# Kernel tuning notes

Measured on AMD Instinct MI355X. Metric: run time of the kernel, lower is better.

The kernel has to match this reference:

```python
import jax, jax.numpy as jnp
import numpy as np

NUM_ROUTES = 12800   # 32 * 20 * 20
NUM_CAPS = 25
IN_CH = 8
OUT_CH = 64
BATCH = 8
NUM_ITERS = 3


def setup_inputs() -> dict:
    key = jax.random.key(0)
    kx, kw = jax.random.split(key)
    x = jax.random.normal(kx, (BATCH, NUM_ROUTES, IN_CH), dtype=jnp.float32)
    # W parameter: torch shape [1, R, C, O, I] -> store as [R, C, O, I]
    W = jax.random.normal(kw, (NUM_ROUTES, NUM_CAPS, OUT_CH, IN_CH), dtype=jnp.float32)
    return {"x": x, "W": W}


def _squash_elementwise(s):
    # Faithful to source: squared_norm sums over last dim of s_j which has size 1,
    # so squash acts elementwise: s^2 * s / ((1+s^2) * |s|) = s*|s|/(1+s^2).
    sq = s * s
    return sq * s / ((1.0 + sq) * jnp.sqrt(sq))


def reference(x, W):
    # u_hat[b,r,c,o] = sum_i W[r,c,o,i] * x[b,r,i]
    u_hat = jnp.einsum('rcoi,bri->brco', W, x)  # [B, R, C, O]
    b_ij = jnp.zeros((NUM_ROUTES, NUM_CAPS), dtype=x.dtype)
    v = None
    for it in range(NUM_ITERS):
        # legacy F.softmax on 4D [1,R,C,1] uses implicit dim=1 -> over routes
        c_ij = jax.nn.softmax(b_ij, axis=0)                  # [R, C]
        s = jnp.einsum('rc,brco->bco', c_ij, u_hat)          # [B, C, O]
        v = _squash_elementwise(s)
        if it < NUM_ITERS - 1:
            # agreement: <u_hat, v> per (b,r,c), then mean over batch
            a = jnp.einsum('brco,bco->brc', u_hat, v)
            b_ij = b_ij + jnp.mean(a, axis=0)
    # torch returns v_j.squeeze(1) with shape [B, C, O, 1]
    return v[..., None]
```

## Files before the change

kernel.cpp:

```cpp
#include <hip/hip_runtime.h>
#include <cstdint>
#include <cstddef>

#define RN 12800
#define CN 25
#define ON 64
#define IN_ 8
#define BN 8
#define SOUT (BN*CN*ON)

#define RPC 64
#define NRC (RN / RPC)
#define NFIN (BN * CN)

typedef float    f4x __attribute__((ext_vector_type(4)));
typedef uint32_t u4x __attribute__((ext_vector_type(4)));

__device__ __forceinline__ uint32_t pack_bf16(float a, float b) {
    uint32_t ua = __float_as_uint(a);
    uint32_t ub = __float_as_uint(b);
    ua = (ua + 0x7fffu + ((ua >> 16) & 1u)) >> 16;
    ub = (ub + 0x7fffu + ((ub >> 16) & 1u)) & 0xffff0000u;
    return ua | ub;
}
__device__ __forceinline__ float lo_bf16(uint32_t q) { return __uint_as_float(q << 16); }
__device__ __forceinline__ float hi_bf16(uint32_t q) { return __uint_as_float(q & 0xffff0000u); }
__device__ __forceinline__ float squashf(float s) { return s * fabsf(s) / (1.f + s * s); }

__global__ void __launch_bounds__(320, 6)
caps_pass0(const float* __restrict__ x, const float* __restrict__ W,
           float* __restrict__ Sp, uint32_t* __restrict__ U)
{
    __shared__ float xs[RPC][BN][IN_];
    const int chunk = blockIdx.y;
    const int r0 = chunk * RPC;

    for (int t = threadIdx.x; t < RPC * BN * 2; t += 320) {
        const int i4 = t & 1;
        const int rl = (t >> 1) & (RPC - 1);
        const int b  = t >> 7;
        const float4 val = *reinterpret_cast<const float4*>(
            x + (((size_t)b * RN + r0 + rl) * IN_) + i4 * 4);
        *reinterpret_cast<float4*>(&xs[rl][b][i4 * 4]) = val;
    }
    __syncthreads();

    const int wave = threadIdx.x >> 6;
    const int lane = threadIdx.x & 63;
    const int c = blockIdx.x * 5 + wave;

    float acc[BN];
    #pragma unroll
    for (int b = 0; b < BN; ++b) acc[b] = 0.f;

    #pragma unroll 2
    for (int rl = 0; rl < RPC; ++rl) {
        const int r = r0 + rl;
        const f4x* wp = reinterpret_cast<const f4x*>(
            W + ((((size_t)r * CN + c) * ON + lane) * IN_));
        const f4x w0 = __builtin_nontemporal_load(wp);
        const f4x w1 = __builtin_nontemporal_load(wp + 1);

        float u[BN];
        #pragma unroll
        for (int b = 0; b < BN; ++b) {
            const float4 xa = *reinterpret_cast<const float4*>(&xs[rl][b][0]);
            const float4 xb = *reinterpret_cast<const float4*>(&xs[rl][b][4]);
            u[b] = w0.x*xa.x + w0.y*xa.y + w0.z*xa.z + w0.w*xa.w
                 + w1.x*xb.x + w1.y*xb.y + w1.z*xb.z + w1.w*xb.w;
            acc[b] += u[b];
        }
        u4x q;
        q.x = pack_bf16(u[0], u[1]);
        q.y = pack_bf16(u[2], u[3]);
        q.z = pack_bf16(u[4], u[5]);
        q.w = pack_bf16(u[6], u[7]);
        __builtin_nontemporal_store(q, reinterpret_cast<u4x*>(
            U + (((size_t)r * CN + c) * ON + lane) * 4));
    }

    float* sp = Sp + (size_t)chunk * SOUT;
    #pragma unroll
    for (int b = 0; b < BN; ++b)
        sp[(b * CN + c) * ON + lane] = acc[b];
}

template<int MODE>
__global__ void __launch_bounds__(320, 6)
caps_passU(const uint32_t* __restrict__ U, const float* __restrict__ vin,
           const float* __restrict__ bin, float* __restrict__ bout,
           float* __restrict__ Sp, float* __restrict__ Zp)
{
    const int chunk = blockIdx.y;
    const int r0 = chunk * RPC;
    const int wave = threadIdx.x >> 6;
    const int lane = threadIdx.x & 63;
    const int c = blockIdx.x * 5 + wave;

    float vreg[BN];
    #pragma unroll
    for (int b = 0; b < BN; ++b)
        vreg[b] = vin[(b * CN + c) * ON + lane];

    float acc[BN];
    #pragma unroll
    for (int b = 0; b < BN; ++b) acc[b] = 0.f;
    float zacc = 0.f;

    #pragma unroll 2
    for (int rl = 0; rl < RPC; ++rl) {
        const int r = r0 + rl;
        const u4x q = __builtin_nontemporal_load(reinterpret_cast<const u4x*>(
            U + (((size_t)r * CN + c) * ON + lane) * 4));
        float u[BN];
        u[0] = lo_bf16(q.x); u[1] = hi_bf16(q.x);
        u[2] = lo_bf16(q.y); u[3] = hi_bf16(q.y);
        u[4] = lo_bf16(q.z); u[5] = hi_bf16(q.z);
        u[6] = lo_bf16(q.w); u[7] = hi_bf16(q.w);

        float p = 0.f;
        #pragma unroll
        for (int b = 0; b < BN; ++b) p += u[b] * vreg[b];
        #pragma unroll
        for (int off = 32; off > 0; off >>= 1) p += __shfl_xor(p, off, 64);

        float bn = p * (1.0f / BN);
        if (MODE == 2) bn += bin[(size_t)r * CN + c];
        if (MODE == 1 && lane == 0) bout[(size_t)r * CN + c] = bn;
        const float e = __expf(bn);
        zacc += e;
        #pragma unroll
        for (int b = 0; b < BN; ++b) acc[b] += e * u[b];
    }

    float* sp = Sp + (size_t)chunk * SOUT;
    #pragma unroll
    for (int b = 0; b < BN; ++b)
        sp[(b * CN + c) * ON + lane] = acc[b];
    if (lane == 0)
        Zp[chunk * 32 + c] = zacc;
}

template<int PASS>
__global__ void __launch_bounds__(320)
caps_fin(const float* __restrict__ Sp, const float* __restrict__ Zp,
         float* __restrict__ vout)
{
    __shared__ float red[320];
    const int wu = blockIdx.x;
    const int t = threadIdx.x, lane = t & 63, g = t >> 6;
    const int c = wu % CN;

    float z = (float)RN;
    if (PASS >= 1) {
        float zp = 0.f;
        for (int j = lane; j < NRC; j += 64) zp += Zp[j * 32 + c];
        #pragma unroll
        for (int off = 32; off > 0; off >>= 1) zp += __shfl_xor(zp, off, 64);
        z = zp;
    }
    const int base = wu * ON + lane;
    float s = 0.f;
    for (int ch = g * 40; ch < g * 40 + 40; ++ch)
        s += Sp[(size_t)ch * SOUT + base];
    red[t] = s;
    __syncthreads();
    if (g == 0) {
        float ss = red[lane] + red[64 + lane] + red[128 + lane]
                 + red[192 + lane] + red[256 + lane];
        ss /= z;
        vout[base] = squashf(ss);
    }
}

extern "C" void kernel_launch(void* const* d_in, const int* in_sizes, int n_in,
                              void* d_out, int out_size, void* d_ws, size_t ws_size,
                              hipStream_t stream)
{
    const float* x = (const float*)d_in[0];
    const float* W = (const float*)d_in[1];
    float* out = (float*)d_out;
    float* ws = (float*)d_ws;

    float* v  = ws;
    float* b1 = v + SOUT;
    float* Zp = b1 + (size_t)RN * CN;
    float* Sp = Zp + (size_t)NRC * 32;
    uint32_t* U = (uint32_t*)(Sp + (size_t)NRC * SOUT);

    dim3 blk(320), grid(5, NRC), fg(NFIN);

    caps_pass0<<<grid, blk, 0, stream>>>(x, W, Sp, U);
    caps_fin<0><<<fg, blk, 0, stream>>>(Sp, Zp, v);
    caps_passU<1><<<grid, blk, 0, stream>>>(U, v, nullptr, b1, Sp, Zp);
    caps_fin<1><<<fg, blk, 0, stream>>>(Sp, Zp, v);
    caps_passU<2><<<grid, blk, 0, stream>>>(U, v, b1, nullptr, Sp, Zp);
    caps_fin<2><<<fg, blk, 0, stream>>>(Sp, Zp, out);
}
```

Measured before the change: 360.3 us.

## Make U capsule-major and batch four route loads per iteration

Reorders the bf16 u_hat intermediate so it is indexed capsule-major ([C][R][O]) instead of route-major. Each wave's sweep over consecutive routes then reads contiguous memory. Both the producing and consuming kernels now issue four route loads up front before computing, to raise memory-level parallelism. The pass0 occupancy hint drops from 6 to 4 waves per SIMD to make room for the extra registers, which may reduce latency hiding.

```diff
diff --git a/kernel.cpp b/kernel.cpp
--- a/kernel.cpp
+++ b/kernel.cpp
@@ -27,7 +27,9 @@
 __device__ __forceinline__ float hi_bf16(uint32_t q) { return __uint_as_float(q & 0xffff0000u); }
 __device__ __forceinline__ float squashf(float s) { return s * fabsf(s) / (1.f + s * s); }
 
-__global__ void __launch_bounds__(320, 6)
+#define UIDX(c, r, lane) ((((size_t)(c) * RN + (r)) * ON + (lane)) * 4)
+
+__global__ void __launch_bounds__(320, 4)
 caps_pass0(const float* __restrict__ x, const float* __restrict__ W,
            float* __restrict__ Sp, uint32_t* __restrict__ U)
 {
@@ -53,30 +55,40 @@
     #pragma unroll
     for (int b = 0; b < BN; ++b) acc[b] = 0.f;
 
-    #pragma unroll 2
-    for (int rl = 0; rl < RPC; ++rl) {
-        const int r = r0 + rl;
-        const f4x* wp = reinterpret_cast<const f4x*>(
-            W + ((((size_t)r * CN + c) * ON + lane) * IN_));
-        const f4x w0 = __builtin_nontemporal_load(wp);
-        const f4x w1 = __builtin_nontemporal_load(wp + 1);
-
-        float u[BN];
-        #pragma unroll
-        for (int b = 0; b < BN; ++b) {
-            const float4 xa = *reinterpret_cast<const float4*>(&xs[rl][b][0]);
-            const float4 xb = *reinterpret_cast<const float4*>(&xs[rl][b][4]);
-            u[b] = w0.x*xa.x + w0.y*xa.y + w0.z*xa.z + w0.w*xa.w
-                 + w1.x*xb.x + w1.y*xb.y + w1.z*xb.z + w1.w*xb.w;
-            acc[b] += u[b];
-        }
-        u4x q;
-        q.x = pack_bf16(u[0], u[1]);
-        q.y = pack_bf16(u[2], u[3]);
-        q.z = pack_bf16(u[4], u[5]);
-        q.w = pack_bf16(u[6], u[7]);
-        __builtin_nontemporal_store(q, reinterpret_cast<u4x*>(
-            U + (((size_t)r * CN + c) * ON + lane) * 4));
+    for (int rg = 0; rg < RPC; rg += 4) {
+        f4x wv[8];
+        #pragma unroll
+        for (int j = 0; j < 4; ++j) {
+            const int r = r0 + rg + j;
+            const f4x* wp = reinterpret_cast<const f4x*>(
+                W + ((((size_t)r * CN + c) * ON + lane) * IN_));
+            wv[2 * j]     = __builtin_nontemporal_load(wp);
+            wv[2 * j + 1] = __builtin_nontemporal_load(wp + 1);
+        }
+        u4x qv[4];
+        #pragma unroll
+        for (int j = 0; j < 4; ++j) {
+            const int rl = rg + j;
+            float u[BN];
+            #pragma unroll
+            for (int b = 0; b < BN; ++b) {
+                const float4 xa = *reinterpret_cast<const float4*>(&xs[rl][b][0]);
+                const float4 xb = *reinterpret_cast<const float4*>(&xs[rl][b][4]);
+                u[b] = wv[2*j].x*xa.x + wv[2*j].y*xa.y + wv[2*j].z*xa.z + wv[2*j].w*xa.w
+                     + wv[2*j+1].x*xb.x + wv[2*j+1].y*xb.y + wv[2*j+1].z*xb.z + wv[2*j+1].w*xb.w;
+                acc[b] += u[b];
+            }
+            qv[j].x = pack_bf16(u[0], u[1]);
+            qv[j].y = pack_bf16(u[2], u[3]);
+            qv[j].z = pack_bf16(u[4], u[5]);
+            qv[j].w = pack_bf16(u[6], u[7]);
+        }
+        #pragma unroll
+        for (int j = 0; j < 4; ++j) {
+            const int r = r0 + rg + j;
+            __builtin_nontemporal_store(qv[j],
+                reinterpret_cast<u4x*>(U + UIDX(c, r, lane)));
+        }
     }
 
     float* sp = Sp + (size_t)chunk * SOUT;
@@ -107,30 +119,36 @@
     for (int b = 0; b < BN; ++b) acc[b] = 0.f;
     float zacc = 0.f;
 
-    #pragma unroll 2
-    for (int rl = 0; rl < RPC; ++rl) {
-        const int r = r0 + rl;
-        const u4x q = __builtin_nontemporal_load(reinterpret_cast<const u4x*>(
-            U + (((size_t)r * CN + c) * ON + lane) * 4));
-        float u[BN];
-        u[0] = lo_bf16(q.x); u[1] = hi_bf16(q.x);
-        u[2] = lo_bf16(q.y); u[3] = hi_bf16(q.y);
-        u[4] = lo_bf16(q.z); u[5] = hi_bf16(q.z);
-        u[6] = lo_bf16(q.w); u[7] = hi_bf16(q.w);
-
-        float p = 0.f;
-        #pragma unroll
-        for (int b = 0; b < BN; ++b) p += u[b] * vreg[b];
-        #pragma unroll
-        for (int off = 32; off > 0; off >>= 1) p += __shfl_xor(p, off, 64);
-
-        float bn = p * (1.0f / BN);
-        if (MODE == 2) bn += bin[(size_t)r * CN + c];
-        if (MODE == 1 && lane == 0) bout[(size_t)r * CN + c] = bn;
-        const float e = __expf(bn);
-        zacc += e;
-        #pragma unroll
-        for (int b = 0; b < BN; ++b) acc[b] += e * u[b];
+    for (int rg = 0; rg < RPC; rg += 4) {
+        u4x qv[4];
+        #pragma unroll
+        for (int j = 0; j < 4; ++j)
+            qv[j] = __builtin_nontemporal_load(reinterpret_cast<const u4x*>(
+                U + UIDX(c, r0 + rg + j, lane)));
+
+        #pragma unroll
+        for (int j = 0; j < 4; ++j) {
+            const int r = r0 + rg + j;
+            float u[BN];
+            u[0] = lo_bf16(qv[j].x); u[1] = hi_bf16(qv[j].x);
+            u[2] = lo_bf16(qv[j].y); u[3] = hi_bf16(qv[j].y);
+            u[4] = lo_bf16(qv[j].z); u[5] = hi_bf16(qv[j].z);
+            u[6] = lo_bf16(qv[j].w); u[7] = hi_bf16(qv[j].w);
+
+            float p = 0.f;
+            #pragma unroll
+            for (int b = 0; b < BN; ++b) p += u[b] * vreg[b];
+            #pragma unroll
+            for (int off = 32; off > 0; off >>= 1) p += __shfl_xor(p, off, 64);
+
+            float bn = p * (1.0f / BN);
+            if (MODE == 2) bn += bin[(size_t)r * CN + c];
+            if (MODE == 1 && lane == 0) bout[(size_t)r * CN + c] = bn;
+            const float e = __expf(bn);
+            zacc += e;
+            #pragma unroll
+            for (int b = 0; b < BN; ++b) acc[b] += e * u[b];
+        }
     }
 
     float* sp = Sp + (size_t)chunk * SOUT;
```

New measurement: 485.9 us. +34.8%, slower.
